# Optimization experiments

Hardware: AMD Instinct MI355X
Metric: run time of the kernel (lower is better)

Reference implementation:

```python
import jax, jax.numpy as jnp
import numpy as np

N_NODES = 150000   # node_num
N_CENTROIDS = 256  # in_feats (must equal out_feats per source view())
EMBED = 256        # out_feats
EPS = 1e-7


def setup_inputs() -> dict:
    key = jax.random.key(0)
    k1, k2, k3 = jax.random.split(key, 3)
    x = jax.random.normal(k1, (N_NODES, EMBED), dtype=jnp.float32)
    # project node representations strictly inside the unit Poincare ball
    x = x / (1.0 + jnp.linalg.norm(x, axis=-1, keepdims=True)) * 0.9
    mask = (jax.random.uniform(k2, (N_NODES, 1)) < 0.9).astype(jnp.float32)
    # centroid_embedding init: uniform(-0.01, 0.01), already well inside the ball
    w = jax.random.uniform(k3, (N_CENTROIDS, EMBED), minval=-0.01, maxval=0.01,
                           dtype=jnp.float32)
    return {"node_repr": x, "mask": mask, "centroid_weight": w}


def _poincare_pairwise(x, c):
    # x: [N, D] inside unit ball, c: [C, D] inside unit ball -> [N, C]
    sx = jnp.sum(x * x, axis=-1)              # [N]
    sc = jnp.sum(c * c, axis=-1)              # [C]
    xc = x @ c.T                               # [N, C] (the only GEMM)
    sq = jnp.maximum(sx[:, None] + sc[None, :] - 2.0 * xc, 0.0)  # ||x-y||^2
    denom = jnp.maximum((1.0 - sx)[:, None] * (1.0 - sc)[None, :], 1e-12)
    arg = 1.0 + 2.0 * sq / denom
    return jnp.arccosh(jnp.maximum(arg, 1.0 + EPS))


def reference(node_repr, mask, centroid_weight):
    # node_repr: [N, D], mask: [N, 1], centroid_weight: [C, D]
    d = _poincare_pairwise(node_repr, centroid_weight)     # [N, C]
    node_centroid_dist = d[None, :, :] * mask              # [1, N, C] (mask broadcasts)
    graph_centroid_dist = jnp.sum(node_centroid_dist, axis=1) / jnp.sum(mask)  # [1, C]
    return graph_centroid_dist, node_centroid_dist
```

## Files before the change

kernel.cpp:

```cpp
#include <hip/hip_runtime.h>
#include <hip/hip_bf16.h>

#define N_NODES 150000
#define CDIM 256
#define DIM 256
#define BM 32

typedef float f32x4 __attribute__((ext_vector_type(4)));
typedef short bf16x8 __attribute__((ext_vector_type(8)));
typedef unsigned short u16x4 __attribute__((ext_vector_type(4)));

#define WS_CB 0
#define WS_SC 131072
#define WS_RC2 132096
#define WS_GACC 133120
#define WS_MSUM 134144

__device__ __forceinline__ unsigned short f2bf(float f) {
  unsigned u = __float_as_uint(f);
  u += 0x7FFFu + ((u >> 16) & 1u);
  return (unsigned short)(u >> 16);
}

__global__ void cd_prep(const float* __restrict__ cw, const float* __restrict__ mask,
                        unsigned short* __restrict__ cb, float* __restrict__ sc,
                        float* __restrict__ rc2, float* __restrict__ msum) {
  int b = blockIdx.x;
  int t = threadIdx.x;
  int wave = t >> 6, lane = t & 63;
  __shared__ float red[4];
  if (b < CDIM) {
    float v = cw[b * DIM + t];
    cb[(size_t)(t >> 3) * (CDIM * 8) + b * 8 + (t & 7)] = f2bf(v);
    float ss = v * v;
    #pragma unroll
    for (int off = 32; off >= 1; off >>= 1) ss += __shfl_xor(ss, off);
    if (lane == 0) red[wave] = ss;
    __syncthreads();
    if (t == 0) {
      float s = red[0] + red[1] + red[2] + red[3];
      sc[b] = s;
      rc2[b] = 2.0f / (1.0f - s);
    }
  } else {
    int idx = (b - CDIM) * 256 + t;
    const int stride = 64 * 256;
    float s = 0.f;
    for (int i = idx; i < N_NODES; i += stride) s += mask[i];
    #pragma unroll
    for (int off = 32; off >= 1; off >>= 1) s += __shfl_xor(s, off);
    if (lane == 0) red[wave] = s;
    __syncthreads();
    if (t == 0) atomicAdd(msum, red[0] + red[1] + red[2] + red[3]);
  }
}

__global__ __launch_bounds__(256, 4)
void cd_main(const float* __restrict__ x, const float* __restrict__ mask,
             const unsigned short* __restrict__ cb, const float* __restrict__ sc,
             const float* __restrict__ rc2, float* __restrict__ gacc,
             float* __restrict__ out1) {
  __shared__ unsigned short ab[32 * BM * 8];
  __shared__ float sxl[BM];
  __shared__ float mskl[BM];

  const int t = threadIdx.x;
  const long m0 = (long)blockIdx.x * BM;

  {
    const int row = t >> 3;
    const int sub = t & 7;
    const long grow = m0 + row;
    const bool ok = grow < N_NODES;
    const float* px = x + grow * DIM + sub * 4;
    f32x4 v[8];
    #pragma unroll
    for (int i = 0; i < 8; ++i)
      v[i] = ok ? *(const f32x4*)(px + i * 32) : f32x4{0.f, 0.f, 0.f, 0.f};
    float ss = 0.f;
    #pragma unroll
    for (int i = 0; i < 8; ++i) {
      ss = fmaf(v[i].x, v[i].x, ss); ss = fmaf(v[i].y, v[i].y, ss);
      ss = fmaf(v[i].z, v[i].z, ss); ss = fmaf(v[i].w, v[i].w, ss);
      u16x4 b;
      b[0] = f2bf(v[i].x); b[1] = f2bf(v[i].y);
      b[2] = f2bf(v[i].z); b[3] = f2bf(v[i].w);
      const int kf = (sub >> 1) + i * 4;
      *(u16x4*)(ab + ((size_t)kf * BM + row) * 8 + (sub & 1) * 4) = b;
    }
    ss += __shfl_xor(ss, 1);
    ss += __shfl_xor(ss, 2);
    ss += __shfl_xor(ss, 4);
    if (sub == 0) {
      sxl[row] = ss;
      mskl[row] = ok ? mask[grow] : 0.f;
    }
  }
  __syncthreads();

  const int lane = t & 63;
  const int w = t >> 6;
  const int q = lane >> 4;
  const int ln = lane & 15;
  const int c0 = w * 64;

  bf16x8 bfc[4], bfn[4];
  #pragma unroll
  for (int nt = 0; nt < 4; ++nt)
    bfc[nt] = *(const bf16x8*)(cb + (size_t)q * (CDIM * 8) + (c0 + nt * 16 + ln) * 8);

  f32x4 acc[2][4] = {};
  #pragma unroll
  for (int kt = 0; kt < 8; ++kt) {
    if (kt < 7) {
      #pragma unroll
      for (int nt = 0; nt < 4; ++nt)
        bfn[nt] = *(const bf16x8*)(cb + (size_t)((kt + 1) * 4 + q) * (CDIM * 8) + (c0 + nt * 16 + ln) * 8);
    }
    bf16x8 af0 = *(const bf16x8*)(ab + ((size_t)(kt * 4 + q) * BM + ln) * 8);
    bf16x8 af1 = *(const bf16x8*)(ab + ((size_t)(kt * 4 + q) * BM + 16 + ln) * 8);
    #pragma unroll
    for (int nt = 0; nt < 4; ++nt)
      acc[0][nt] = __builtin_amdgcn_mfma_f32_16x16x32_bf16(af0, bfc[nt], acc[0][nt], 0, 0, 0);
    #pragma unroll
    for (int nt = 0; nt < 4; ++nt)
      acc[1][nt] = __builtin_amdgcn_mfma_f32_16x16x32_bf16(af1, bfc[nt], acc[1][nt], 0, 0, 0);
    if (kt < 7) {
      #pragma unroll
      for (int nt = 0; nt < 4; ++nt) bfc[nt] = bfn[nt];
    }
  }

  float scv[4], rc2v[4];
  #pragma unroll
  for (int nt = 0; nt < 4; ++nt) {
    scv[nt] = sc[c0 + nt * 16 + ln];
    rc2v[nt] = rc2[c0 + nt * 16 + ln];
  }

  float pc[4] = {0.f, 0.f, 0.f, 0.f};
  #pragma unroll
  for (int mt = 0; mt < 2; ++mt) {
    float sxe[4], rxi[4], mke[4];
    long rows[4];
    #pragma unroll
    for (int i = 0; i < 4; ++i) {
      const int rloc = mt * 16 + q * 4 + i;
      sxe[i] = sxl[rloc];
      rows[i] = m0 + rloc;
      mke[i] = mskl[rloc] * 0.6931471805599453f;
      rxi[i] = __builtin_amdgcn_rcpf(1.0f - sxe[i]);
    }
    #pragma unroll
    for (int nt = 0; nt < 4; ++nt) {
      const int col = c0 + nt * 16 + ln;
      #pragma unroll
      for (int i = 0; i < 4; ++i) {
        float xc = acc[mt][nt][i];
        float sq = fmaxf(fmaf(-2.0f, xc, sxe[i] + scv[nt]), 0.0f);
        float z = fmaf(sq * rxi[i], rc2v[nt], 1.0f);
        z = fmaxf(z, 1.0f + 1e-7f);
        float t2 = z + sqrtf(fmaf(z, z, -1.0f));
        float o = __log2f(t2) * mke[i];
        if (rows[i] < N_NODES) out1[rows[i] * CDIM + col] = o;
        pc[nt] += o;
      }
    }
  }

  #pragma unroll
  for (int nt = 0; nt < 4; ++nt) {
    float s = pc[nt];
    s += __shfl_xor(s, 16);
    s += __shfl_xor(s, 32);
    if (lane < 16) atomicAdd(gacc + c0 + nt * 16 + ln, s);
  }
}

__global__ void cd_final(const float* __restrict__ gacc, const float* __restrict__ msum,
                         float* __restrict__ out0) {
  int t = threadIdx.x;
  out0[t] = gacc[t] / msum[0];
}

extern "C" void kernel_launch(void* const* d_in, const int* in_sizes, int n_in,
                              void* d_out, int out_size, void* d_ws, size_t ws_size,
                              hipStream_t stream) {
  const float* x    = (const float*)d_in[0];
  const float* mask = (const float*)d_in[1];
  const float* cw   = (const float*)d_in[2];
  float* out = (float*)d_out;
  char* ws = (char*)d_ws;
  unsigned short* cb = (unsigned short*)(ws + WS_CB);
  float* sc   = (float*)(ws + WS_SC);
  float* rc2  = (float*)(ws + WS_RC2);
  float* gacc = (float*)(ws + WS_GACC);
  float* msum = (float*)(ws + WS_MSUM);

  hipMemsetAsync(ws + WS_GACC, 0, 256 * 4 + 4, stream);
  cd_prep<<<320, 256, 0, stream>>>(cw, mask, cb, sc, rc2, msum);
  const int nblocks = (N_NODES + BM - 1) / BM;
  cd_main<<<nblocks, 256, 0, stream>>>(x, mask, cb, sc, rc2, gacc, out + 256);
  cd_final<<<1, 256, 0, stream>>>(gacc, msum, out);
}
```

Before: 340.3 us.

## Make main kernel persistent with prefetch of next tile and swizzled LDS

Turns cd_main into a persistent grid of 1024 blocks that loop over 32-row tiles, prefetching the next tile's node rows into registers while the current tile's MFMA and epilogue run. The shared-memory staging now uses 8-wide bf16 stores with an XOR swizzle to reduce bank conflicts. Per-column atomics are spread over 64 replicated accumulators, which the final kernel sums. This aims to hide global load latency and cut atomic contention, but adds a sync per tile, more register pressure and lower parallelism than the old one-tile-per-block grid.

Result: slower. 431.0 us (+26.6%).

```diff
diff --git a/kernel.cpp b/kernel.cpp
--- a/kernel.cpp
+++ b/kernel.cpp
@@ -5,16 +5,20 @@
 #define CDIM 256
 #define DIM 256
 #define BM 32
+#define NT 4688
+#define GRID 1024
 
 typedef float f32x4 __attribute__((ext_vector_type(4)));
 typedef short bf16x8 __attribute__((ext_vector_type(8)));
-typedef unsigned short u16x4 __attribute__((ext_vector_type(4)));
+typedef unsigned short u16x8 __attribute__((ext_vector_type(8)));
 
 #define WS_CB 0
 #define WS_SC 131072
 #define WS_RC2 132096
-#define WS_GACC 133120
-#define WS_MSUM 134144
+#define WS_MSUM 133120
+#define WS_GACCR 133632
+#define WS_ZERO_FROM 133120
+#define WS_ZERO_LEN (133632 + 65536 - 133120)
 
 __device__ __forceinline__ unsigned short f2bf(float f) {
   unsigned u = __float_as_uint(f);
@@ -58,78 +62,58 @@
 __global__ __launch_bounds__(256, 4)
 void cd_main(const float* __restrict__ x, const float* __restrict__ mask,
              const unsigned short* __restrict__ cb, const float* __restrict__ sc,
-             const float* __restrict__ rc2, float* __restrict__ gacc,
+             const float* __restrict__ rc2, float* __restrict__ gaccR,
              float* __restrict__ out1) {
   __shared__ unsigned short ab[32 * BM * 8];
   __shared__ float sxl[BM];
   __shared__ float mskl[BM];
 
   const int t = threadIdx.x;
-  const long m0 = (long)blockIdx.x * BM;
-
-  {
-    const int row = t >> 3;
-    const int sub = t & 7;
-    const long grow = m0 + row;
-    const bool ok = grow < N_NODES;
-    const float* px = x + grow * DIM + sub * 4;
-    f32x4 v[8];
-    #pragma unroll
-    for (int i = 0; i < 8; ++i)
-      v[i] = ok ? *(const f32x4*)(px + i * 32) : f32x4{0.f, 0.f, 0.f, 0.f};
-    float ss = 0.f;
-    #pragma unroll
-    for (int i = 0; i < 8; ++i) {
-      ss = fmaf(v[i].x, v[i].x, ss); ss = fmaf(v[i].y, v[i].y, ss);
-      ss = fmaf(v[i].z, v[i].z, ss); ss = fmaf(v[i].w, v[i].w, ss);
-      u16x4 b;
-      b[0] = f2bf(v[i].x); b[1] = f2bf(v[i].y);
-      b[2] = f2bf(v[i].z); b[3] = f2bf(v[i].w);
-      const int kf = (sub >> 1) + i * 4;
-      *(u16x4*)(ab + ((size_t)kf * BM + row) * 8 + (sub & 1) * 4) = b;
-    }
-    ss += __shfl_xor(ss, 1);
-    ss += __shfl_xor(ss, 2);
-    ss += __shfl_xor(ss, 4);
-    if (sub == 0) {
-      sxl[row] = ss;
-      mskl[row] = ok ? mask[grow] : 0.f;
-    }
-  }
-  __syncthreads();
-
+  const int bid = blockIdx.x;
   const int lane = t & 63;
   const int w = t >> 6;
   const int q = lane >> 4;
   const int ln = lane & 15;
   const int c0 = w * 64;
-
-  bf16x8 bfc[4], bfn[4];
-  #pragma unroll
-  for (int nt = 0; nt < 4; ++nt)
-    bfc[nt] = *(const bf16x8*)(cb + (size_t)q * (CDIM * 8) + (c0 + nt * 16 + ln) * 8);
-
-  f32x4 acc[2][4] = {};
-  #pragma unroll
-  for (int kt = 0; kt < 8; ++kt) {
-    if (kt < 7) {
-      #pragma unroll
-      for (int nt = 0; nt < 4; ++nt)
-        bfn[nt] = *(const bf16x8*)(cb + (size_t)((kt + 1) * 4 + q) * (CDIM * 8) + (c0 + nt * 16 + ln) * 8);
-    }
-    bf16x8 af0 = *(const bf16x8*)(ab + ((size_t)(kt * 4 + q) * BM + ln) * 8);
-    bf16x8 af1 = *(const bf16x8*)(ab + ((size_t)(kt * 4 + q) * BM + 16 + ln) * 8);
-    #pragma unroll
-    for (int nt = 0; nt < 4; ++nt)
-      acc[0][nt] = __builtin_amdgcn_mfma_f32_16x16x32_bf16(af0, bfc[nt], acc[0][nt], 0, 0, 0);
-    #pragma unroll
-    for (int nt = 0; nt < 4; ++nt)
-      acc[1][nt] = __builtin_amdgcn_mfma_f32_16x16x32_bf16(af1, bfc[nt], acc[1][nt], 0, 0, 0);
-    if (kt < 7) {
-      #pragma unroll
-      for (int nt = 0; nt < 4; ++nt) bfc[nt] = bfn[nt];
-    }
-  }
+  const int srow = t >> 3;
+  const int sub  = t & 7;
+
+  f32x4 va[4], vb[4];
+  float mreg;
+
+  {
+    long grow = (long)bid * BM + srow;
+    bool ok = grow < N_NODES;
+    const float* px = x + grow * DIM + sub * 8;
+    #pragma unroll
+    for (int i = 0; i < 4; ++i) {
+      va[i] = ok ? *(const f32x4*)(px + i * 64) : f32x4{0.f, 0.f, 0.f, 0.f};
+      vb[i] = ok ? *(const f32x4*)(px + i * 64 + 4) : f32x4{0.f, 0.f, 0.f, 0.f};
+    }
+    mreg = ok ? mask[grow] : 0.f;
+  }
+  {
+    float ss = 0.f;
+    #pragma unroll
+    for (int i = 0; i < 4; ++i) {
+      ss = fmaf(va[i].x, va[i].x, ss); ss = fmaf(va[i].y, va[i].y, ss);
+      ss = fmaf(va[i].z, va[i].z, ss); ss = fmaf(va[i].w, va[i].w, ss);
+      ss = fmaf(vb[i].x, vb[i].x, ss); ss = fmaf(vb[i].y, vb[i].y, ss);
+      ss = fmaf(vb[i].z, vb[i].z, ss); ss = fmaf(vb[i].w, vb[i].w, ss);
+      u16x8 bpk;
+      bpk[0] = f2bf(va[i].x); bpk[1] = f2bf(va[i].y);
+      bpk[2] = f2bf(va[i].z); bpk[3] = f2bf(va[i].w);
+      bpk[4] = f2bf(vb[i].x); bpk[5] = f2bf(vb[i].y);
+      bpk[6] = f2bf(vb[i].z); bpk[7] = f2bf(vb[i].w);
+      const int kf = sub + 8 * i;
+      *(u16x8*)(ab + (((kf * BM + srow) * 8) ^ (sub << 3))) = bpk;
+    }
+    ss += __shfl_xor(ss, 1);
+    ss += __shfl_xor(ss, 2);
+    ss += __shfl_xor(ss, 4);
+    if (sub == 0) { sxl[srow] = ss; mskl[srow] = mreg; }
+  }
+  __syncthreads();
 
   float scv[4], rc2v[4];
   #pragma unroll
@@ -139,48 +123,120 @@
   }
 
   float pc[4] = {0.f, 0.f, 0.f, 0.f};
-  #pragma unroll
-  for (int mt = 0; mt < 2; ++mt) {
-    float sxe[4], rxi[4], mke[4];
-    long rows[4];
-    #pragma unroll
-    for (int i = 0; i < 4; ++i) {
-      const int rloc = mt * 16 + q * 4 + i;
-      sxe[i] = sxl[rloc];
-      rows[i] = m0 + rloc;
-      mke[i] = mskl[rloc] * 0.6931471805599453f;
-      rxi[i] = __builtin_amdgcn_rcpf(1.0f - sxe[i]);
-    }
-    #pragma unroll
-    for (int nt = 0; nt < 4; ++nt) {
-      const int col = c0 + nt * 16 + ln;
+
+  for (long tt = bid; tt < NT; tt += GRID) {
+    const long tn = tt + GRID;
+    const bool have_next = tn < NT;
+
+    f32x4 acc[2][4] = {};
+    bf16x8 bfc[4], bfn[4];
+    #pragma unroll
+    for (int nt = 0; nt < 4; ++nt)
+      bfc[nt] = *(const bf16x8*)(cb + (size_t)q * (CDIM * 8) + (c0 + nt * 16 + ln) * 8);
+    #pragma unroll
+    for (int kt = 0; kt < 8; ++kt) {
+      if (kt < 7) {
+        #pragma unroll
+        for (int nt = 0; nt < 4; ++nt)
+          bfn[nt] = *(const bf16x8*)(cb + (size_t)((kt + 1) * 4 + q) * (CDIM * 8) + (c0 + nt * 16 + ln) * 8);
+      }
+      const int kf = kt * 4 + q;
+      bf16x8 af0 = *(const bf16x8*)(ab + (((kf * BM + ln) * 8) ^ ((kf & 7) << 3)));
+      bf16x8 af1 = *(const bf16x8*)(ab + (((kf * BM + 16 + ln) * 8) ^ ((kf & 7) << 3)));
+      #pragma unroll
+      for (int nt = 0; nt < 4; ++nt)
+        acc[0][nt] = __builtin_amdgcn_mfma_f32_16x16x32_bf16(af0, bfc[nt], acc[0][nt], 0, 0, 0);
+      #pragma unroll
+      for (int nt = 0; nt < 4; ++nt)
+        acc[1][nt] = __builtin_amdgcn_mfma_f32_16x16x32_bf16(af1, bfc[nt], acc[1][nt], 0, 0, 0);
+      if (kt < 7) {
+        #pragma unroll
+        for (int nt = 0; nt < 4; ++nt) bfc[nt] = bfn[nt];
+      }
+    }
+
+    if (have_next) {
+      long grow = tn * BM + srow;
+      bool ok = grow < N_NODES;
+      const float* px = x + grow * DIM + sub * 8;
       #pragma unroll
       for (int i = 0; i < 4; ++i) {
-        float xc = acc[mt][nt][i];
-        float sq = fmaxf(fmaf(-2.0f, xc, sxe[i] + scv[nt]), 0.0f);
-        float z = fmaf(sq * rxi[i], rc2v[nt], 1.0f);
-        z = fmaxf(z, 1.0f + 1e-7f);
-        float t2 = z + sqrtf(fmaf(z, z, -1.0f));
-        float o = __log2f(t2) * mke[i];
-        if (rows[i] < N_NODES) out1[rows[i] * CDIM + col] = o;
-        pc[nt] += o;
-      }
-    }
-  }
-
+        va[i] = ok ? *(const f32x4*)(px + i * 64) : f32x4{0.f, 0.f, 0.f, 0.f};
+        vb[i] = ok ? *(const f32x4*)(px + i * 64 + 4) : f32x4{0.f, 0.f, 0.f, 0.f};
+      }
+      mreg = ok ? mask[grow] : 0.f;
+    }
+
+    #pragma unroll
+    for (int mt = 0; mt < 2; ++mt) {
+      float sxe[4], rxi[4], mke[4];
+      long rows[4];
+      #pragma unroll
+      for (int i = 0; i < 4; ++i) {
+        const int rloc = mt * 16 + q * 4 + i;
+        sxe[i] = sxl[rloc];
+        rows[i] = tt * BM + rloc;
+        mke[i] = mskl[rloc] * 0.6931471805599453f;
+        rxi[i] = __builtin_amdgcn_rcpf(1.0f - sxe[i]);
+      }
+      #pragma unroll
+      for (int nt = 0; nt < 4; ++nt) {
+        const int col = c0 + nt * 16 + ln;
+        #pragma unroll
+        for (int i = 0; i < 4; ++i) {
+          float xc = acc[mt][nt][i];
+          float sq = fmaxf(fmaf(-2.0f, xc, sxe[i] + scv[nt]), 0.0f);
+          float z = fmaf(sq * rxi[i], rc2v[nt], 1.0f);
+          z = fmaxf(z, 1.0f + 1e-7f);
+          float t2 = z + sqrtf(fmaf(z, z, -1.0f));
+          float o = __log2f(t2) * mke[i];
+          if (rows[i] < N_NODES) out1[rows[i] * CDIM + col] = o;
+          pc[nt] += o;
+        }
+      }
+    }
+
+    __syncthreads();
+    if (have_next) {
+      float ss = 0.f;
+      #pragma unroll
+      for (int i = 0; i < 4; ++i) {
+        ss = fmaf(va[i].x, va[i].x, ss); ss = fmaf(va[i].y, va[i].y, ss);
+        ss = fmaf(va[i].z, va[i].z, ss); ss = fmaf(va[i].w, va[i].w, ss);
+        ss = fmaf(vb[i].x, vb[i].x, ss); ss = fmaf(vb[i].y, vb[i].y, ss);
+        ss = fmaf(vb[i].z, vb[i].z, ss); ss = fmaf(vb[i].w, vb[i].w, ss);
+        u16x8 bpk;
+        bpk[0] = f2bf(va[i].x); bpk[1] = f2bf(va[i].y);
+        bpk[2] = f2bf(va[i].z); bpk[3] = f2bf(va[i].w);
+        bpk[4] = f2bf(vb[i].x); bpk[5] = f2bf(vb[i].y);
+        bpk[6] = f2bf(vb[i].z); bpk[7] = f2bf(vb[i].w);
+        const int kf = sub + 8 * i;
+        *(u16x8*)(ab + (((kf * BM + srow) * 8) ^ (sub << 3))) = bpk;
+      }
+      ss += __shfl_xor(ss, 1);
+      ss += __shfl_xor(ss, 2);
+      ss += __shfl_xor(ss, 4);
+      if (sub == 0) { sxl[srow] = ss; mskl[srow] = mreg; }
+      __syncthreads();
+    }
+  }
+
+  float* gr = gaccR + (size_t)(bid & 63) * CDIM;
   #pragma unroll
   for (int nt = 0; nt < 4; ++nt) {
     float s = pc[nt];
     s += __shfl_xor(s, 16);
     s += __shfl_xor(s, 32);
-    if (lane < 16) atomicAdd(gacc + c0 + nt * 16 + ln, s);
-  }
-}
-
-__global__ void cd_final(const float* __restrict__ gacc, const float* __restrict__ msum,
+    if (lane < 16) atomicAdd(gr + c0 + nt * 16 + ln, s);
+  }
+}
+
+__global__ void cd_final(const float* __restrict__ gaccR, const float* __restrict__ msum,
                          float* __restrict__ out0) {
   int t = threadIdx.x;
-  out0[t] = gacc[t] / msum[0];
+  float s = 0.f;
+  for (int r = 0; r < 64; ++r) s += gaccR[r * CDIM + t];
+  out0[t] = s / msum[0];
 }
 
 extern "C" void kernel_launch(void* const* d_in, const int* in_sizes, int n_in,
@@ -192,14 +248,13 @@
   float* out = (float*)d_out;
   char* ws = (char*)d_ws;
   unsigned short* cb = (unsigned short*)(ws + WS_CB);
-  float* sc   = (float*)(ws + WS_SC);
-  float* rc2  = (float*)(ws + WS_RC2);
-  float* gacc = (float*)(ws + WS_GACC);
-  float* msum = (float*)(ws + WS_MSUM);
-
-  hipMemsetAsync(ws + WS_GACC, 0, 256 * 4 + 4, stream);
+  float* sc    = (float*)(ws + WS_SC);
+  float* rc2   = (float*)(ws + WS_RC2);
+  float* msum  = (float*)(ws + WS_MSUM);
+  float* gaccR = (float*)(ws + WS_GACCR);
+
+  hipMemsetAsync(ws + WS_ZERO_FROM, 0, WS_ZERO_LEN, stream);
   cd_prep<<<320, 256, 0, stream>>>(cw, mask, cb, sc, rc2, msum);
-  const int nblocks = (N_NODES + BM - 1) / BM;
-  cd_main<<<nblocks, 256, 0, stream>>>(x, mask, cb, sc, rc2, gacc, out + 256);
-  cd_final<<<1, 256, 0, stream>>>(gacc, msum, out);
-}
+  cd_main<<<GRID, 256, 0, stream>>>(x, mask, cb, sc, rc2, gaccR, out + 256);
+  cd_final<<<1, 256, 0, stream>>>(gaccR, msum, out);
+}
```
